# Optimization experiments

Measured on AMD Instinct MI355X. Metric: run time of the kernel, lower is better.

The kernel has to match this reference:

```python
import jax, jax.numpy as jnp
import numpy as np

B, D, O = 16384, 1024, 2048
MU, LAM = 0.9, 0.1


def setup_inputs() -> dict:
    key = jax.random.key(0)
    ks = jax.random.split(key, 16)
    stdv = float(1.0 / np.sqrt(D))
    u = lambda k, shape, s: jax.random.uniform(k, shape, jnp.float32, -s, s)
    return {
        "x": jax.random.normal(ks[0], (B, D), jnp.float32),
        "x_ctx": jax.random.normal(ks[1], (B, D), jnp.float32),
        "classifier": u(ks[2], (O, D), stdv),
        "none_tensor": u(ks[3], (1, D), stdv),
        "ctx_q_w": u(ks[4], (O, D), stdv),
        "ctx_q_b": u(ks[5], (O,), stdv),
        "word_g_w": u(ks[6], (1, D), stdv),
        "word_g_b": u(ks[7], (1,), stdv),
        "tcq_w1": u(ks[8], (D, D), stdv),
        "tcq_b1": u(ks[9], (D,), stdv),
        "tcq_w2": u(ks[10], (O, D), stdv),
        "tcq_b2": u(ks[11], (O,), stdv),
        "history_input": 0.1 * jax.random.normal(ks[12], (O - 1, D), jnp.float32),
        "history_count": jax.random.randint(ks[13], (O - 1,), 0, 10),
        "labels": jax.random.randint(ks[14], (B,), 0, O),
    }


def reference(x, x_ctx, classifier, none_tensor, ctx_q_w, ctx_q_b,
              word_g_w, word_g_b, tcq_w1, tcq_b1, tcq_w2, tcq_b2,
              history_input, history_count, labels):
    mu, lam = MU, LAM
    # ---- update_history (torch.no_grad), vectorized over classes via segment_sum ----
    xs = jax.lax.stop_gradient(x)
    sums = jax.ops.segment_sum(xs, labels, num_segments=O)               # [O, D]
    counts = jax.ops.segment_sum(jnp.ones((B,), jnp.float32), labels, num_segments=O)  # [O]
    has = counts[1:] > 0                                                  # classes 1..O-1
    cls_mean = sums[1:] / jnp.maximum(counts[1:], 1.0)[:, None]
    hist = jnp.where(has[:, None], mu * history_input + cls_mean, history_input)
    cnt = history_count + has.astype(history_count.dtype)
    # ---- generate_substitute (mu < 1 branch) ----
    denom = 1.0 - jnp.power(mu, jnp.maximum(cnt, 1).astype(jnp.float32))[:, None]
    v = hist * (1.0 - mu) / denom                                        # [O-1, D]
    r_sub = jnp.concatenate([none_tensor, v], axis=0)                    # [O, D]
    ctx_logits = x_ctx @ ctx_q_w.T + ctx_q_b                              # [B, O]
    att_logits = jax.nn.gelu(x @ tcq_w1.T + tcq_b1, approximate=False) @ tcq_w2.T + tcq_b2  # [B, O]
    # ---- gated combine + bilinear classifier (training=True path: w uses ctx_logits) ----
    g_word = jax.nn.sigmoid(x @ word_g_w.T + word_g_b)                    # [B, 1]
    w = g_word * jax.nn.sigmoid(ctx_logits)                               # [B, O]
    # logits = sum(((1-w)*x[:,None,:] + w*r_sub) * classifier, -1), collapsed algebraically
    logits = (1.0 - w) * (x @ classifier.T) + w * jnp.einsum('od,od->o', r_sub, classifier)[None, :]
    # ---- losses on labels >= 0 (mask-weighted means, jit-safe) ----
    mask = (labels >= 0).astype(jnp.float32)
    n = jnp.maximum(mask.sum(), 1.0)
    lsm = jax.nn.log_softmax(logits, axis=-1)
    nll = -jnp.take_along_axis(lsm, jnp.maximum(labels, 0)[:, None], axis=1)[:, 0]
    ce = (mask * nll).sum() / n
    mse_row = jnp.mean((ctx_logits - att_logits) ** 2, axis=-1)
    mse = (mask * mse_row).sum() / n
    return (ce + lam * mse, logits)
```

## Files before the change

kernel.cpp:

```cpp
#include <hip/hip_runtime.h>
#include <cstdint>
#include <cstddef>

#define DEV __device__ __forceinline__

typedef __attribute__((ext_vector_type(4))) float f32x4;
typedef __attribute__((ext_vector_type(8))) short bf16x8;
typedef unsigned short ushort_t;
typedef __attribute__((ext_vector_type(8))) unsigned short ushort8;

static constexpr int B_ = 16384, D_ = 1024, O_ = 2048;
static constexpr float LAM_ = 0.1f;

static constexpr size_t WS_XBF   = 0;
static constexpr size_t WS_XCBF  = WS_XBF   + (size_t)B_ * D_ * 2;
static constexpr size_t WS_HBF   = WS_XCBF  + (size_t)B_ * D_ * 2;
static constexpr size_t WS_CLSBF = WS_HBF   + (size_t)B_ * D_ * 2;
static constexpr size_t WS_CTWBF = WS_CLSBF + (size_t)O_ * D_ * 2;
static constexpr size_t WS_W2BF  = WS_CTWBF + (size_t)O_ * D_ * 2;
static constexpr size_t WS_W1BF  = WS_W2BF  + (size_t)O_ * D_ * 2;
static constexpr size_t WS_SMALL = WS_W1BF  + (size_t)D_ * D_ * 2;
static constexpr size_t SM_COUNTS = 0;
static constexpr size_t SM_TSUM   = 8192;
static constexpr size_t SM_MSE    = 16384;
static constexpr size_t SM_ZERO_BYTES = 82176;
static constexpr size_t SM_S      = 82176;
static constexpr size_t SM_GWORD  = 90368;
static constexpr size_t SM_CEROW  = 155904;

DEV float wave_sum(float v) {
  #pragma unroll
  for (int o = 32; o; o >>= 1) v += __shfl_xor(v, o, 64);
  return v;
}

DEV ushort_t f2bf1(float f) {
  union { float f; unsigned u; } c{f};
  unsigned r = c.u + 0x7fffu + ((c.u >> 16) & 1u);
  return (ushort_t)(r >> 16);
}

DEV float sigmoidf(float z) { return 1.0f / (1.0f + expf(-z)); }

DEV void gload_lds16(const ushort_t* g, ushort_t* l) {
  __builtin_amdgcn_global_load_lds((const __attribute__((address_space(1))) void*)g,
                                   (__attribute__((address_space(3))) void*)l, 16, 0, 0);
}

DEV void stage2(const ushort_t* __restrict__ s0, ushort_t* slot, int tid) {
  gload_lds16(s0, slot + tid * 8);
  gload_lds16(s0 + 128 * 1024, slot + (tid + 512) * 8);
}

DEV f32x4 mfma16(bf16x8 a, bf16x8 b, f32x4 c) {
  return __builtin_amdgcn_mfma_f32_16x16x32_bf16(a, b, c, 0, 0, 0);
}

#define DSR(dst, addr, off) \
  asm volatile("ds_read_b128 %0, %1 offset:" off : "=v"(dst) : "v"(addr))

__global__ __launch_bounds__(256) void f2bf_kernel(const float* __restrict__ in,
                                                   ushort_t* __restrict__ out, int n8) {
  int i = blockIdx.x * 256 + threadIdx.x;
  if (i >= n8) return;
  const float4* p = (const float4*)(in + (size_t)i * 8);
  float4 a = p[0], b = p[1];
  ushort8 o;
  o[0] = f2bf1(a.x); o[1] = f2bf1(a.y); o[2] = f2bf1(a.z); o[3] = f2bf1(a.w);
  o[4] = f2bf1(b.x); o[5] = f2bf1(b.y); o[6] = f2bf1(b.z); o[7] = f2bf1(b.w);
  *(ushort8*)(out + (size_t)i * 8) = o;
}

__global__ __launch_bounds__(256) void rowdot_kernel(const float* __restrict__ x,
    const float* __restrict__ cls, const float* __restrict__ wg,
    const float* __restrict__ wgb, const int* __restrict__ labels,
    float* __restrict__ tsum, float* __restrict__ counts, float* __restrict__ g_word) {
  int wave = threadIdx.x >> 6, lane = threadIdx.x & 63;
  int row = blockIdx.x * 4 + wave;
  const float* xr = x + (size_t)row * D_;
  int lab = labels[row];
  const float* cr = cls + (size_t)max(lab, 0) * D_;
  float t = 0.f, g = 0.f;
  #pragma unroll
  for (int j = 0; j < 4; ++j) {
    int d = j * 256 + lane * 4;
    float4 xv = *(const float4*)(xr + d);
    float4 cv = *(const float4*)(cr + d);
    float4 wv = *(const float4*)(wg + d);
    t += xv.x * cv.x + xv.y * cv.y + xv.z * cv.z + xv.w * cv.w;
    g += xv.x * wv.x + xv.y * wv.y + xv.z * wv.z + xv.w * wv.w;
  }
  t = wave_sum(t); g = wave_sum(g);
  if (lane == 0) {
    if (lab >= 0) {
      atomicAdd(&tsum[lab], t);
      atomicAdd(&counts[lab], 1.0f);
    }
    g_word[row] = sigmoidf(g + wgb[0]);
  }
}

__global__ __launch_bounds__(256) void scls_kernel(const float* __restrict__ cls,
    const float* __restrict__ none_t, const float* __restrict__ hist,
    const int* __restrict__ hcnt, const float* __restrict__ counts,
    const float* __restrict__ tsum, float* __restrict__ s) {
  int wave = threadIdx.x >> 6, lane = threadIdx.x & 63;
  int o = blockIdx.x * 4 + wave;
  if (o >= O_) return;
  const float* cr = cls + (size_t)o * D_;
  const float* src = (o == 0) ? none_t : hist + (size_t)(o - 1) * D_;
  float dv = 0.f;
  #pragma unroll
  for (int j = 0; j < 4; ++j) {
    int d = j * 256 + lane * 4;
    float4 a = *(const float4*)(src + d);
    float4 c = *(const float4*)(cr + d);
    dv += a.x * c.x + a.y * c.y + a.z * c.z + a.w * c.w;
  }
  dv = wave_sum(dv);
  if (lane == 0) {
    if (o == 0) { s[0] = dv; }
    else {
      float co = counts[o];
      bool has = co > 0.f;
      int cnt = hcnt[o - 1] + (has ? 1 : 0);
      float denom = 1.f - powf(0.9f, (float)max(cnt, 1));
      float val = has ? (0.9f * dv + tsum[o] / fmaxf(co, 1.f)) : dv;
      s[o] = (0.1f / denom) * val;
    }
  }
}

template<bool S01, bool S23, int W1, int W3>
DEV void tile8(int t, const ushort_t* __restrict__ sA0, const ushort_t* __restrict__ sB0,
               ushort_t* lds, int tid, unsigned aoffB, unsigned boffB, f32x4 (&acc)[8][4]) {
  const unsigned s0 = (unsigned)(((2 * t) & 3) * 16384);
  const unsigned s1 = (unsigned)(((2 * t + 1) & 3) * 16384);
  unsigned aA0 = aoffB + s0, aB0 = boffB + 65536u + s0;
  unsigned aA1 = aoffB + s1, aB1 = boffB + 65536u + s1;
  bf16x8 afr[4], bfr[4];
  DSR(bfr[0], aB0, "0"); DSR(bfr[1], aB0, "1024"); DSR(bfr[2], aB0, "2048"); DSR(bfr[3], aB0, "3072");
  DSR(afr[0], aA0, "0"); DSR(afr[1], aA0, "1024"); DSR(afr[2], aA0, "2048"); DSR(afr[3], aA0, "3072");
  if constexpr (S01) stage2(sA0 + (size_t)(2 * t + 3) * 32, lds + ((2 * t + 3) & 3) * 8192, tid);
  __builtin_amdgcn_s_barrier();
  asm volatile("s_waitcnt lgkmcnt(0)");
  __builtin_amdgcn_sched_barrier(0);
  __builtin_amdgcn_s_setprio(1);
  #pragma unroll
  for (int m = 0; m < 4; m++)
    #pragma unroll
    for (int n = 0; n < 4; n++) acc[m][n] = mfma16(afr[m], bfr[n], acc[m][n]);
  __builtin_amdgcn_s_setprio(0);
  __builtin_amdgcn_s_barrier();
  DSR(afr[0], aA0, "4096"); DSR(afr[1], aA0, "5120"); DSR(afr[2], aA0, "6144"); DSR(afr[3], aA0, "7168");
  if constexpr (S01) stage2(sB0 + (size_t)(2 * t + 3) * 32, lds + 32768 + ((2 * t + 3) & 3) * 8192, tid);
  __builtin_amdgcn_s_barrier();
  asm volatile("s_waitcnt lgkmcnt(0)");
  __builtin_amdgcn_sched_barrier(0);
  __builtin_amdgcn_s_setprio(1);
  #pragma unroll
  for (int m = 0; m < 4; m++)
    #pragma unroll
    for (int n = 0; n < 4; n++) acc[m + 4][n] = mfma16(afr[m], bfr[n], acc[m + 4][n]);
  __builtin_amdgcn_s_setprio(0);
  if constexpr (W1 == 8) asm volatile("s_waitcnt vmcnt(8)" ::: "memory");
  else if constexpr (W1 == 4) asm volatile("s_waitcnt vmcnt(4)" ::: "memory");
  else if constexpr (W1 == 0) asm volatile("s_waitcnt vmcnt(0)" ::: "memory");
  __builtin_amdgcn_s_barrier();
  DSR(bfr[0], aB1, "0"); DSR(bfr[1], aB1, "1024"); DSR(bfr[2], aB1, "2048"); DSR(bfr[3], aB1, "3072");
  DSR(afr[0], aA1, "0"); DSR(afr[1], aA1, "1024"); DSR(afr[2], aA1, "2048"); DSR(afr[3], aA1, "3072");
  if constexpr (S23) stage2(sA0 + (size_t)(2 * t + 4) * 32, lds + ((2 * t + 4) & 3) * 8192, tid);
  __builtin_amdgcn_s_barrier();
  asm volatile("s_waitcnt lgkmcnt(0)");
  __builtin_amdgcn_sched_barrier(0);
  __builtin_amdgcn_s_setprio(1);
  #pragma unroll
  for (int m = 0; m < 4; m++)
    #pragma unroll
    for (int n = 0; n < 4; n++) acc[m][n] = mfma16(afr[m], bfr[n], acc[m][n]);
  __builtin_amdgcn_s_setprio(0);
  __builtin_amdgcn_s_barrier();
  DSR(afr[0], aA1, "4096"); DSR(afr[1], aA1, "5120"); DSR(afr[2], aA1, "6144"); DSR(afr[3], aA1, "7168");
  if constexpr (S23) stage2(sB0 + (size_t)(2 * t + 4) * 32, lds + 32768 + ((2 * t + 4) & 3) * 8192, tid);
  __builtin_amdgcn_s_barrier();
  asm volatile("s_waitcnt lgkmcnt(0)");
  __builtin_amdgcn_sched_barrier(0);
  __builtin_amdgcn_s_setprio(1);
  #pragma unroll
  for (int m = 0; m < 4; m++)
    #pragma unroll
    for (int n = 0; n < 4; n++) acc[m + 4][n] = mfma16(afr[m], bfr[n], acc[m + 4][n]);
  __builtin_amdgcn_s_setprio(0);
  if constexpr (W3 == 8) asm volatile("s_waitcnt vmcnt(8)" ::: "memory");
  else if constexpr (W3 == 4) asm volatile("s_waitcnt vmcnt(4)" ::: "memory");
  else if constexpr (W3 == 2) asm volatile("s_waitcnt vmcnt(2)" ::: "memory");
  else if constexpr (W3 == 0) asm volatile("s_waitcnt vmcnt(0)" ::: "memory");
  __builtin_amdgcn_s_barrier();
}

template<int EPI, int NTSHIFT>
__global__ __launch_bounds__(512, 2) void gemm8_kernel(
    const ushort_t* __restrict__ A, const ushort_t* __restrict__ Bmat,
    const float* __restrict__ bias, float* __restrict__ fout,
    ushort_t* __restrict__ hout, const float* __restrict__ g_word,
    const float* __restrict__ svec, float* __restrict__ mse_row) {
  __shared__ __align__(16) ushort_t lds[65536];
  const int tid = threadIdx.x, lane = tid & 63, wave = tid >> 6;
  const int wr = wave >> 2, wc = wave & 3;
  const int nwg = 64 << NTSHIFT, cpx = nwg >> 3;
  int bid = blockIdx.x;
  int wg = (bid & 7) * cpx + (bid >> 3);
  const int bm = wg >> NTSHIFT, bn = wg & ((1 << NTSHIFT) - 1);
  const int NCOL = 256 << NTSHIFT;
  const int qsrc = (tid & 3) ^ ((tid >> 3) & 3);
  const ushort_t* sA0 = A + ((size_t)bm * 256 + (tid >> 2)) * 1024 + qsrc * 8;
  const ushort_t* sB0 = Bmat + ((size_t)bn * 256 + (tid >> 2)) * 1024 + qsrc * 8;
  const int qrd = (lane >> 4) ^ (((lane & 15) >> 1) & 3);
  const unsigned aoffB = (unsigned)(((wr * 128 + (lane & 15)) * 32 + qrd * 8) * 2);
  const unsigned boffB = (unsigned)(((wc * 64 + (lane & 15)) * 32 + qrd * 8) * 2);
  f32x4 acc[8][4] = {};
  stage2(sA0, lds, tid);
  stage2(sB0, lds + 32768, tid);
  stage2(sA0 + 32, lds + 8192, tid);
  stage2(sB0 + 32, lds + 32768 + 8192, tid);
  stage2(sA0 + 64, lds + 2 * 8192, tid);
  stage2(sB0 + 64, lds + 32768 + 2 * 8192, tid);
  asm volatile("s_waitcnt vmcnt(8)" ::: "memory");
  __builtin_amdgcn_s_barrier();
  for (int t = 0; t < 14; ++t)
    tile8<true, true, 8, 8>(t, sA0, sB0, lds, tid, aoffB, boffB, acc);
  tile8<true, false, 8, 4>(14, sA0, sB0, lds, tid, aoffB, boffB, acc);
  tile8<false, false, 0, 0>(15, sA0, sB0, lds, tid, aoffB, boffB, acc);
  #pragma unroll
  for (int m = 0; m < 8; m++) {
    #pragma unroll
    for (int i = 0; i < 4; i++) {
      int row = bm * 256 + wr * 128 + m * 16 + (lane >> 4) * 4 + i;
      float gw = 0.f, msum = 0.f;
      if constexpr (EPI == 3) gw = g_word[row];
      #pragma unroll
      for (int n = 0; n < 4; n++) {
        int col = bn * 256 + wc * 64 + n * 16 + (lane & 15);
        float v = acc[m][n][i];
        if constexpr (EPI == 0) {
          float z = v + bias[col];
          float gl = 0.5f * z * (1.f + erff(z * 0.70710678118f));
          hout[(size_t)row * 1024 + col] = f2bf1(gl);
        } else if constexpr (EPI == 1) {
          fout[(size_t)row * NCOL + col] = v + bias[col];
        } else if constexpr (EPI == 2) {
          float att = v + bias[col];
          float ctx = fout[(size_t)row * NCOL + col];
          float d = ctx - att;
          msum += d * d;
        } else {
          size_t off = (size_t)row * NCOL + col;
          float ctx = fout[off];
          float w = gw * sigmoidf(ctx);
          fout[off] = (1.f - w) * v + w * svec[col];
        }
      }
      if constexpr (EPI == 2) {
        #pragma unroll
        for (int o = 1; o < 16; o <<= 1) msum += __shfl_xor(msum, o, 64);
        if ((lane & 15) == 0) atomicAdd(&mse_row[row], msum);
      }
    }
  }
}

__global__ __launch_bounds__(256) void ce_kernel(const float* __restrict__ logits,
    const int* __restrict__ labels, float* __restrict__ ce_row) {
  int row = blockIdx.x, t = threadIdx.x, lane = t & 63, wave = t >> 6;
  const float* lr = logits + (size_t)row * O_;
  float v[8];
  float m = -INFINITY;
  #pragma unroll
  for (int j = 0; j < 8; j++) { v[j] = lr[t + j * 256]; m = fmaxf(m, v[j]); }
  #pragma unroll
  for (int o = 32; o; o >>= 1) m = fmaxf(m, __shfl_xor(m, o, 64));
  __shared__ float red[8];
  if (lane == 0) red[wave] = m;
  __syncthreads();
  m = fmaxf(fmaxf(red[0], red[1]), fmaxf(red[2], red[3]));
  float se = 0.f;
  #pragma unroll
  for (int j = 0; j < 8; j++) se += expf(v[j] - m);
  se = wave_sum(se);
  if (lane == 0) red[4 + wave] = se;
  __syncthreads();
  if (t == 0) {
    float bs = red[4] + red[5] + red[6] + red[7];
    int lab = labels[row];
    float nll = 0.f;
    if (lab >= 0) nll = -(lr[lab] - m - logf(bs));
    ce_row[row] = nll;
  }
}

__global__ __launch_bounds__(256) void finalize_kernel(const float* __restrict__ ce_row,
    const float* __restrict__ mse_row, const int* __restrict__ labels,
    float* __restrict__ out0) {
  int t = threadIdx.x, lane = t & 63, wave = t >> 6;
  float sn = 0.f, sm = 0.f, sc = 0.f;
  for (int i = t; i < B_; i += 256) {
    if (labels[i] >= 0) { sn += ce_row[i]; sm += mse_row[i]; sc += 1.f; }
  }
  sn = wave_sum(sn); sm = wave_sum(sm); sc = wave_sum(sc);
  __shared__ float r0[4], r1[4], r2[4];
  if (lane == 0) { r0[wave] = sn; r1[wave] = sm; r2[wave] = sc; }
  __syncthreads();
  if (t == 0) {
    float a = r0[0] + r0[1] + r0[2] + r0[3];
    float b = r1[0] + r1[1] + r1[2] + r1[3];
    float c = r2[0] + r2[1] + r2[2] + r2[3];
    out0[0] = (a + LAM_ * (b / (float)O_)) / fmaxf(c, 1.f);
  }
}

extern "C" void kernel_launch(void* const* d_in, const int* in_sizes, int n_in,
                              void* d_out, int out_size, void* d_ws, size_t ws_size,
                              hipStream_t stream) {
  const float* x        = (const float*)d_in[0];
  const float* x_ctx    = (const float*)d_in[1];
  const float* cls      = (const float*)d_in[2];
  const float* none_t   = (const float*)d_in[3];
  const float* ctx_q_w  = (const float*)d_in[4];
  const float* ctx_q_b  = (const float*)d_in[5];
  const float* word_g_w = (const float*)d_in[6];
  const float* word_g_b = (const float*)d_in[7];
  const float* w1       = (const float*)d_in[8];
  const float* b1       = (const float*)d_in[9];
  const float* w2       = (const float*)d_in[10];
  const float* b2       = (const float*)d_in[11];
  const float* hist     = (const float*)d_in[12];
  const int*   hcnt     = (const int*)d_in[13];
  const int*   labels   = (const int*)d_in[14];

  float* out  = (float*)d_out;
  float* out1 = out + 1;
  char* ws = (char*)d_ws;

  ushort_t* xbf   = (ushort_t*)(ws + WS_XBF);
  ushort_t* xcbf  = (ushort_t*)(ws + WS_XCBF);
  ushort_t* hbf   = (ushort_t*)(ws + WS_HBF);
  ushort_t* clsbf = (ushort_t*)(ws + WS_CLSBF);
  ushort_t* ctwbf = (ushort_t*)(ws + WS_CTWBF);
  ushort_t* w2bf  = (ushort_t*)(ws + WS_W2BF);
  ushort_t* w1bf  = (ushort_t*)(ws + WS_W1BF);
  float* counts   = (float*)(ws + WS_SMALL + SM_COUNTS);
  float* tsum     = (float*)(ws + WS_SMALL + SM_TSUM);
  float* mse_row  = (float*)(ws + WS_SMALL + SM_MSE);
  float* s        = (float*)(ws + WS_SMALL + SM_S);
  float* g_word   = (float*)(ws + WS_SMALL + SM_GWORD);
  float* ce_row   = (float*)(ws + WS_SMALL + SM_CEROW);

  hipMemsetAsync(ws + WS_SMALL, 0, SM_ZERO_BYTES, stream);

  f2bf_kernel<<<8192, 256, 0, stream>>>(x, xbf, B_ * D_ / 8);
  f2bf_kernel<<<8192, 256, 0, stream>>>(x_ctx, xcbf, B_ * D_ / 8);
  f2bf_kernel<<<1024, 256, 0, stream>>>(cls, clsbf, O_ * D_ / 8);
  f2bf_kernel<<<1024, 256, 0, stream>>>(ctx_q_w, ctwbf, O_ * D_ / 8);
  f2bf_kernel<<<1024, 256, 0, stream>>>(w2, w2bf, O_ * D_ / 8);
  f2bf_kernel<<<512, 256, 0, stream>>>(w1, w1bf, D_ * D_ / 8);

  rowdot_kernel<<<B_ / 4, 256, 0, stream>>>(x, cls, word_g_w, word_g_b, labels,
                                            tsum, counts, g_word);
  scls_kernel<<<O_ / 4, 256, 0, stream>>>(cls, none_t, hist, hcnt, counts, tsum, s);

  gemm8_kernel<0, 2><<<64 * 4, 512, 0, stream>>>(xbf, w1bf, b1, nullptr, hbf,
                                                 nullptr, nullptr, nullptr);
  gemm8_kernel<1, 3><<<64 * 8, 512, 0, stream>>>(xcbf, ctwbf, ctx_q_b, out1, nullptr,
                                                 nullptr, nullptr, nullptr);
  gemm8_kernel<2, 3><<<64 * 8, 512, 0, stream>>>(hbf, w2bf, b2, out1, nullptr,
                                                 nullptr, nullptr, mse_row);
  gemm8_kernel<3, 3><<<64 * 8, 512, 0, stream>>>(xbf, clsbf, nullptr, out1, nullptr,
                                                 g_word, s, nullptr);

  ce_kernel<<<B_, 256, 0, stream>>>(out1, labels, ce_row);
  finalize_kernel<<<1, 256, 0, stream>>>(ce_row, mse_row, labels, out);
}
```

Measured before the change: 466.8 us.

## Double-buffer LDS fragment registers to overlap ds_reads with MFMA in GEMM

Restructures the GEMM inner loop so LDS fragment reads for the next sub-step are issued before the current MFMA block, using two register buffers for A and B fragments. Partial lgkmcnt waits replace full drains, and one barrier per phase is removed. The vmcnt waits are retuned for the new schedule. This is meant to hide LDS read latency behind matrix math, at the cost of more VGPRs and a more delicate ordering that could hit races or spills.

Result: faster. 455.0 us (-2.5%).

```diff
diff --git a/kernel.cpp b/kernel.cpp
--- a/kernel.cpp
+++ b/kernel.cpp
@@ -59,6 +59,14 @@
 #define DSR(dst, addr, off) \
   asm volatile("ds_read_b128 %0, %1 offset:" off : "=v"(dst) : "v"(addr))
 
+template<int N> DEV void wait_vm() {
+  if constexpr (N == 8)      asm volatile("s_waitcnt vmcnt(8)" ::: "memory");
+  else if constexpr (N == 6) asm volatile("s_waitcnt vmcnt(6)" ::: "memory");
+  else if constexpr (N == 4) asm volatile("s_waitcnt vmcnt(4)" ::: "memory");
+  else if constexpr (N == 2) asm volatile("s_waitcnt vmcnt(2)" ::: "memory");
+  else                       asm volatile("s_waitcnt vmcnt(0)" ::: "memory");
+}
+
 __global__ __launch_bounds__(256) void f2bf_kernel(const float* __restrict__ in,
                                                    ushort_t* __restrict__ out, int n8) {
   int i = blockIdx.x * 256 + threadIdx.x;
@@ -131,70 +139,78 @@
   }
 }
 
-template<bool S01, bool S23, int W1, int W3>
-DEV void tile8(int t, const ushort_t* __restrict__ sA0, const ushort_t* __restrict__ sB0,
-               ushort_t* lds, int tid, unsigned aoffB, unsigned boffB, f32x4 (&acc)[8][4]) {
-  const unsigned s0 = (unsigned)(((2 * t) & 3) * 16384);
-  const unsigned s1 = (unsigned)(((2 * t + 1) & 3) * 16384);
-  unsigned aA0 = aoffB + s0, aB0 = boffB + 65536u + s0;
-  unsigned aA1 = aoffB + s1, aB1 = boffB + 65536u + s1;
-  bf16x8 afr[4], bfr[4];
-  DSR(bfr[0], aB0, "0"); DSR(bfr[1], aB0, "1024"); DSR(bfr[2], aB0, "2048"); DSR(bfr[3], aB0, "3072");
-  DSR(afr[0], aA0, "0"); DSR(afr[1], aA0, "1024"); DSR(afr[2], aA0, "2048"); DSR(afr[3], aA0, "3072");
+template<bool S01, bool S23, int W0, int W1, int W2, int W3, bool RLAST>
+DEV void tile4(int t, const ushort_t* __restrict__ sA0, const ushort_t* __restrict__ sB0,
+               ushort_t* lds, int tid, unsigned aoffB, unsigned boffB,
+               bf16x8 (&bA)[2][4], bf16x8 (&bB)[2][4], f32x4 (&acc)[8][4]) {
+  const unsigned sl0 = (unsigned)(((2 * t) & 3) * 16384);
+  const unsigned sl1 = (unsigned)(((2 * t + 1) & 3) * 16384);
+  const unsigned sl2 = (unsigned)(((2 * t + 2) & 3) * 16384);
+  const unsigned aA0 = aoffB + sl0;
+  const unsigned aA1 = aoffB + sl1, aB1 = boffB + 65536u + sl1;
+  const unsigned aA2 = aoffB + sl2, aB2 = boffB + 65536u + sl2;
+  DSR(bA[1][0], aA0, "4096"); DSR(bA[1][1], aA0, "5120");
+  DSR(bA[1][2], aA0, "6144"); DSR(bA[1][3], aA0, "7168");
   if constexpr (S01) stage2(sA0 + (size_t)(2 * t + 3) * 32, lds + ((2 * t + 3) & 3) * 8192, tid);
-  __builtin_amdgcn_s_barrier();
-  asm volatile("s_waitcnt lgkmcnt(0)");
+  asm volatile("s_waitcnt lgkmcnt(4)");
   __builtin_amdgcn_sched_barrier(0);
   __builtin_amdgcn_s_setprio(1);
   #pragma unroll
   for (int m = 0; m < 4; m++)
     #pragma unroll
-    for (int n = 0; n < 4; n++) acc[m][n] = mfma16(afr[m], bfr[n], acc[m][n]);
+    for (int n = 0; n < 4; n++) acc[m][n] = mfma16(bA[0][m], bB[0][n], acc[m][n]);
   __builtin_amdgcn_s_setprio(0);
+  __builtin_amdgcn_sched_barrier(0);
+  wait_vm<W0>();
   __builtin_amdgcn_s_barrier();
-  DSR(afr[0], aA0, "4096"); DSR(afr[1], aA0, "5120"); DSR(afr[2], aA0, "6144"); DSR(afr[3], aA0, "7168");
+  DSR(bB[1][0], aB1, "0"); DSR(bB[1][1], aB1, "1024");
+  DSR(bB[1][2], aB1, "2048"); DSR(bB[1][3], aB1, "3072");
+  DSR(bA[0][0], aA1, "0"); DSR(bA[0][1], aA1, "1024");
+  DSR(bA[0][2], aA1, "2048"); DSR(bA[0][3], aA1, "3072");
   if constexpr (S01) stage2(sB0 + (size_t)(2 * t + 3) * 32, lds + 32768 + ((2 * t + 3) & 3) * 8192, tid);
-  __builtin_amdgcn_s_barrier();
-  asm volatile("s_waitcnt lgkmcnt(0)");
+  asm volatile("s_waitcnt lgkmcnt(8)");
   __builtin_amdgcn_sched_barrier(0);
   __builtin_amdgcn_s_setprio(1);
   #pragma unroll
   for (int m = 0; m < 4; m++)
     #pragma unroll
-    for (int n = 0; n < 4; n++) acc[m + 4][n] = mfma16(afr[m], bfr[n], acc[m + 4][n]);
+    for (int n = 0; n < 4; n++) acc[m + 4][n] = mfma16(bA[1][m], bB[0][n], acc[m + 4][n]);
   __builtin_amdgcn_s_setprio(0);
-  if constexpr (W1 == 8) asm volatile("s_waitcnt vmcnt(8)" ::: "memory");
-  else if constexpr (W1 == 4) asm volatile("s_waitcnt vmcnt(4)" ::: "memory");
-  else if constexpr (W1 == 0) asm volatile("s_waitcnt vmcnt(0)" ::: "memory");
+  __builtin_amdgcn_sched_barrier(0);
+  wait_vm<W1>();
   __builtin_amdgcn_s_barrier();
-  DSR(bfr[0], aB1, "0"); DSR(bfr[1], aB1, "1024"); DSR(bfr[2], aB1, "2048"); DSR(bfr[3], aB1, "3072");
-  DSR(afr[0], aA1, "0"); DSR(afr[1], aA1, "1024"); DSR(afr[2], aA1, "2048"); DSR(afr[3], aA1, "3072");
+  DSR(bA[1][0], aA1, "4096"); DSR(bA[1][1], aA1, "5120");
+  DSR(bA[1][2], aA1, "6144"); DSR(bA[1][3], aA1, "7168");
   if constexpr (S23) stage2(sA0 + (size_t)(2 * t + 4) * 32, lds + ((2 * t + 4) & 3) * 8192, tid);
-  __builtin_amdgcn_s_barrier();
-  asm volatile("s_waitcnt lgkmcnt(0)");
+  asm volatile("s_waitcnt lgkmcnt(4)");
   __builtin_amdgcn_sched_barrier(0);
   __builtin_amdgcn_s_setprio(1);
   #pragma unroll
   for (int m = 0; m < 4; m++)
     #pragma unroll
-    for (int n = 0; n < 4; n++) acc[m][n] = mfma16(afr[m], bfr[n], acc[m][n]);
+    for (int n = 0; n < 4; n++) acc[m][n] = mfma16(bA[0][m], bB[1][n], acc[m][n]);
   __builtin_amdgcn_s_setprio(0);
+  __builtin_amdgcn_sched_barrier(0);
+  wait_vm<W2>();
   __builtin_amdgcn_s_barrier();
-  DSR(afr[0], aA1, "4096"); DSR(afr[1], aA1, "5120"); DSR(afr[2], aA1, "6144"); DSR(afr[3], aA1, "7168");
+  if constexpr (!RLAST) {
+    DSR(bB[0][0], aB2, "0"); DSR(bB[0][1], aB2, "1024");
+    DSR(bB[0][2], aB2, "2048"); DSR(bB[0][3], aB2, "3072");
+    DSR(bA[0][0], aA2, "0"); DSR(bA[0][1], aA2, "1024");
+    DSR(bA[0][2], aA2, "2048"); DSR(bA[0][3], aA2, "3072");
+  }
   if constexpr (S23) stage2(sB0 + (size_t)(2 * t + 4) * 32, lds + 32768 + ((2 * t + 4) & 3) * 8192, tid);
-  __builtin_amdgcn_s_barrier();
-  asm volatile("s_waitcnt lgkmcnt(0)");
+  if constexpr (RLAST) asm volatile("s_waitcnt lgkmcnt(0)");
+  else                 asm volatile("s_waitcnt lgkmcnt(8)");
   __builtin_amdgcn_sched_barrier(0);
   __builtin_amdgcn_s_setprio(1);
   #pragma unroll
   for (int m = 0; m < 4; m++)
     #pragma unroll
-    for (int n = 0; n < 4; n++) acc[m + 4][n] = mfma16(afr[m], bfr[n], acc[m + 4][n]);
+    for (int n = 0; n < 4; n++) acc[m + 4][n] = mfma16(bA[1][m], bB[1][n], acc[m + 4][n]);
   __builtin_amdgcn_s_setprio(0);
-  if constexpr (W3 == 8) asm volatile("s_waitcnt vmcnt(8)" ::: "memory");
-  else if constexpr (W3 == 4) asm volatile("s_waitcnt vmcnt(4)" ::: "memory");
-  else if constexpr (W3 == 2) asm volatile("s_waitcnt vmcnt(2)" ::: "memory");
-  else if constexpr (W3 == 0) asm volatile("s_waitcnt vmcnt(0)" ::: "memory");
+  __builtin_amdgcn_sched_barrier(0);
+  wait_vm<W3>();
   __builtin_amdgcn_s_barrier();
 }
 
@@ -227,10 +243,18 @@
   stage2(sB0 + 64, lds + 32768 + 2 * 8192, tid);
   asm volatile("s_waitcnt vmcnt(8)" ::: "memory");
   __builtin_amdgcn_s_barrier();
+  bf16x8 bA[2][4], bB[2][4];
+  {
+    const unsigned aB0 = boffB + 65536u;
+    DSR(bB[0][0], aB0, "0"); DSR(bB[0][1], aB0, "1024");
+    DSR(bB[0][2], aB0, "2048"); DSR(bB[0][3], aB0, "3072");
+    DSR(bA[0][0], aoffB, "0"); DSR(bA[0][1], aoffB, "1024");
+    DSR(bA[0][2], aoffB, "2048"); DSR(bA[0][3], aoffB, "3072");
+  }
   for (int t = 0; t < 14; ++t)
-    tile8<true, true, 8, 8>(t, sA0, sB0, lds, tid, aoffB, boffB, acc);
-  tile8<true, false, 8, 4>(14, sA0, sB0, lds, tid, aoffB, boffB, acc);
-  tile8<false, false, 0, 0>(15, sA0, sB0, lds, tid, aoffB, boffB, acc);
+    tile4<true, true, 6, 6, 6, 6, false>(t, sA0, sB0, lds, tid, aoffB, boffB, bA, bB, acc);
+  tile4<true, false, 6, 6, 4, 2, false>(14, sA0, sB0, lds, tid, aoffB, boffB, bA, bB, acc);
+  tile4<false, false, 0, 0, 0, 0, true>(15, sA0, sB0, lds, tid, aoffB, boffB, bA, bB, acc);
   #pragma unroll
   for (int m = 0; m < 8; m++) {
     #pragma unroll
```

## Shrink GEMM tile to 256x128 with 3-stage pipeline for higher occupancy

Applied to the files above, without the earlier changes.

Replaces the 256x256 block tile with a 4-stage LDS ring by a 256x128 tile, 4x2 wave layout and a 3-stage ring of single k-slices. LDS use drops from 128 KB to 72 KB and launch bounds rise to 4 blocks per CU, so more workgroups can overlap and the grids double. The cost is lower arithmetic intensity per tile, since A is reloaded twice as often, and fewer MFMAs between barriers.

Result: slower. 478.4 us (+2.5%).

```diff
diff --git a/kernel.cpp b/kernel.cpp
--- a/kernel.cpp
+++ b/kernel.cpp
@@ -47,11 +47,6 @@
                                    (__attribute__((address_space(3))) void*)l, 16, 0, 0);
 }
 
-DEV void stage2(const ushort_t* __restrict__ s0, ushort_t* slot, int tid) {
-  gload_lds16(s0, slot + tid * 8);
-  gload_lds16(s0 + 128 * 1024, slot + (tid + 512) * 8);
-}
-
 DEV f32x4 mfma16(bf16x8 a, bf16x8 b, f32x4 c) {
   return __builtin_amdgcn_mfma_f32_16x16x32_bf16(a, b, c, 0, 0, 0);
 }
@@ -131,116 +126,77 @@
   }
 }
 
-template<bool S01, bool S23, int W1, int W3>
-DEV void tile8(int t, const ushort_t* __restrict__ sA0, const ushort_t* __restrict__ sB0,
-               ushort_t* lds, int tid, unsigned aoffB, unsigned boffB, f32x4 (&acc)[8][4]) {
-  const unsigned s0 = (unsigned)(((2 * t) & 3) * 16384);
-  const unsigned s1 = (unsigned)(((2 * t + 1) & 3) * 16384);
-  unsigned aA0 = aoffB + s0, aB0 = boffB + 65536u + s0;
-  unsigned aA1 = aoffB + s1, aB1 = boffB + 65536u + s1;
-  bf16x8 afr[4], bfr[4];
-  DSR(bfr[0], aB0, "0"); DSR(bfr[1], aB0, "1024"); DSR(bfr[2], aB0, "2048"); DSR(bfr[3], aB0, "3072");
-  DSR(afr[0], aA0, "0"); DSR(afr[1], aA0, "1024"); DSR(afr[2], aA0, "2048"); DSR(afr[3], aA0, "3072");
-  if constexpr (S01) stage2(sA0 + (size_t)(2 * t + 3) * 32, lds + ((2 * t + 3) & 3) * 8192, tid);
-  __builtin_amdgcn_s_barrier();
-  asm volatile("s_waitcnt lgkmcnt(0)");
-  __builtin_amdgcn_sched_barrier(0);
-  __builtin_amdgcn_s_setprio(1);
-  #pragma unroll
-  for (int m = 0; m < 4; m++)
-    #pragma unroll
-    for (int n = 0; n < 4; n++) acc[m][n] = mfma16(afr[m], bfr[n], acc[m][n]);
-  __builtin_amdgcn_s_setprio(0);
-  __builtin_amdgcn_s_barrier();
-  DSR(afr[0], aA0, "4096"); DSR(afr[1], aA0, "5120"); DSR(afr[2], aA0, "6144"); DSR(afr[3], aA0, "7168");
-  if constexpr (S01) stage2(sB0 + (size_t)(2 * t + 3) * 32, lds + 32768 + ((2 * t + 3) & 3) * 8192, tid);
-  __builtin_amdgcn_s_barrier();
-  asm volatile("s_waitcnt lgkmcnt(0)");
-  __builtin_amdgcn_sched_barrier(0);
-  __builtin_amdgcn_s_setprio(1);
-  #pragma unroll
-  for (int m = 0; m < 4; m++)
-    #pragma unroll
-    for (int n = 0; n < 4; n++) acc[m + 4][n] = mfma16(afr[m], bfr[n], acc[m + 4][n]);
-  __builtin_amdgcn_s_setprio(0);
-  if constexpr (W1 == 8) asm volatile("s_waitcnt vmcnt(8)" ::: "memory");
-  else if constexpr (W1 == 4) asm volatile("s_waitcnt vmcnt(4)" ::: "memory");
-  else if constexpr (W1 == 0) asm volatile("s_waitcnt vmcnt(0)" ::: "memory");
-  __builtin_amdgcn_s_barrier();
-  DSR(bfr[0], aB1, "0"); DSR(bfr[1], aB1, "1024"); DSR(bfr[2], aB1, "2048"); DSR(bfr[3], aB1, "3072");
-  DSR(afr[0], aA1, "0"); DSR(afr[1], aA1, "1024"); DSR(afr[2], aA1, "2048"); DSR(afr[3], aA1, "3072");
-  if constexpr (S23) stage2(sA0 + (size_t)(2 * t + 4) * 32, lds + ((2 * t + 4) & 3) * 8192, tid);
-  __builtin_amdgcn_s_barrier();
-  asm volatile("s_waitcnt lgkmcnt(0)");
-  __builtin_amdgcn_sched_barrier(0);
-  __builtin_amdgcn_s_setprio(1);
-  #pragma unroll
-  for (int m = 0; m < 4; m++)
-    #pragma unroll
-    for (int n = 0; n < 4; n++) acc[m][n] = mfma16(afr[m], bfr[n], acc[m][n]);
-  __builtin_amdgcn_s_setprio(0);
-  __builtin_amdgcn_s_barrier();
-  DSR(afr[0], aA1, "4096"); DSR(afr[1], aA1, "5120"); DSR(afr[2], aA1, "6144"); DSR(afr[3], aA1, "7168");
-  if constexpr (S23) stage2(sB0 + (size_t)(2 * t + 4) * 32, lds + 32768 + ((2 * t + 4) & 3) * 8192, tid);
-  __builtin_amdgcn_s_barrier();
-  asm volatile("s_waitcnt lgkmcnt(0)");
-  __builtin_amdgcn_sched_barrier(0);
-  __builtin_amdgcn_s_setprio(1);
-  #pragma unroll
-  for (int m = 0; m < 4; m++)
-    #pragma unroll
-    for (int n = 0; n < 4; n++) acc[m + 4][n] = mfma16(afr[m], bfr[n], acc[m + 4][n]);
-  __builtin_amdgcn_s_setprio(0);
-  if constexpr (W3 == 8) asm volatile("s_waitcnt vmcnt(8)" ::: "memory");
-  else if constexpr (W3 == 4) asm volatile("s_waitcnt vmcnt(4)" ::: "memory");
-  else if constexpr (W3 == 2) asm volatile("s_waitcnt vmcnt(2)" ::: "memory");
-  else if constexpr (W3 == 0) asm volatile("s_waitcnt vmcnt(0)" ::: "memory");
-  __builtin_amdgcn_s_barrier();
-}
-
-template<int EPI, int NTSHIFT>
-__global__ __launch_bounds__(512, 2) void gemm8_kernel(
+template<int EPI, int NBN>
+__global__ __launch_bounds__(512, 4) void gemm8_kernel(
     const ushort_t* __restrict__ A, const ushort_t* __restrict__ Bmat,
     const float* __restrict__ bias, float* __restrict__ fout,
     ushort_t* __restrict__ hout, const float* __restrict__ g_word,
     const float* __restrict__ svec, float* __restrict__ mse_row) {
-  __shared__ __align__(16) ushort_t lds[65536];
+  __shared__ __align__(16) ushort_t lds[36864];
   const int tid = threadIdx.x, lane = tid & 63, wave = tid >> 6;
-  const int wr = wave >> 2, wc = wave & 3;
-  const int nwg = 64 << NTSHIFT, cpx = nwg >> 3;
+  const int wr = wave >> 1, wc = wave & 1;
+  const int nwg = 64 * NBN, cpx = nwg >> 3;
   int bid = blockIdx.x;
   int wg = (bid & 7) * cpx + (bid >> 3);
-  const int bm = wg >> NTSHIFT, bn = wg & ((1 << NTSHIFT) - 1);
-  const int NCOL = 256 << NTSHIFT;
+  const int bm = wg / NBN, bn = wg % NBN;
+  const int NCOL = NBN * 128;
   const int qsrc = (tid & 3) ^ ((tid >> 3) & 3);
   const ushort_t* sA0 = A + ((size_t)bm * 256 + (tid >> 2)) * 1024 + qsrc * 8;
-  const ushort_t* sB0 = Bmat + ((size_t)bn * 256 + (tid >> 2)) * 1024 + qsrc * 8;
+  const ushort_t* sB0 = Bmat + ((size_t)bn * 128 + (tid >> 2)) * 1024 + qsrc * 8;
   const int qrd = (lane >> 4) ^ (((lane & 15) >> 1) & 3);
-  const unsigned aoffB = (unsigned)(((wr * 128 + (lane & 15)) * 32 + qrd * 8) * 2);
-  const unsigned boffB = (unsigned)(((wc * 64 + (lane & 15)) * 32 + qrd * 8) * 2);
-  f32x4 acc[8][4] = {};
-  stage2(sA0, lds, tid);
-  stage2(sB0, lds + 32768, tid);
-  stage2(sA0 + 32, lds + 8192, tid);
-  stage2(sB0 + 32, lds + 32768 + 8192, tid);
-  stage2(sA0 + 64, lds + 2 * 8192, tid);
-  stage2(sB0 + 64, lds + 32768 + 2 * 8192, tid);
-  asm volatile("s_waitcnt vmcnt(8)" ::: "memory");
+  const unsigned aoffB = (unsigned)(((wr * 64 + (lane & 15)) * 32 + qrd * 8) * 2);
+  const unsigned boffB = (unsigned)(((wc * 64 + (lane & 15)) * 32 + qrd * 8) * 2) + 49152u;
+  f32x4 acc[4][4] = {};
+  gload_lds16(sA0, lds + tid * 8);
+  gload_lds16(sA0 + 128 * 1024, lds + (tid + 512) * 8);
+  gload_lds16(sB0, lds + 24576 + tid * 8);
+  gload_lds16(sA0 + 32, lds + 8192 + tid * 8);
+  gload_lds16(sA0 + 32 + 128 * 1024, lds + 8192 + (tid + 512) * 8);
+  gload_lds16(sB0 + 32, lds + 24576 + 4096 + tid * 8);
+  asm volatile("s_waitcnt vmcnt(3)" ::: "memory");
   __builtin_amdgcn_s_barrier();
-  for (int t = 0; t < 14; ++t)
-    tile8<true, true, 8, 8>(t, sA0, sB0, lds, tid, aoffB, boffB, acc);
-  tile8<true, false, 8, 4>(14, sA0, sB0, lds, tid, aoffB, boffB, acc);
-  tile8<false, false, 0, 0>(15, sA0, sB0, lds, tid, aoffB, boffB, acc);
-  #pragma unroll
-  for (int m = 0; m < 8; m++) {
+  #pragma unroll
+  for (int t = 0; t < 32; ++t) {
+    const unsigned aA = aoffB + (unsigned)((t % 3) * 16384);
+    const unsigned aB = boffB + (unsigned)((t % 3) * 8192);
+    bf16x8 fA[4], fB[4];
+    DSR(fB[0], aB, "0"); DSR(fB[1], aB, "1024");
+    DSR(fB[2], aB, "2048"); DSR(fB[3], aB, "3072");
+    DSR(fA[0], aA, "0"); DSR(fA[1], aA, "1024");
+    DSR(fA[2], aA, "2048"); DSR(fA[3], aA, "3072");
+    if (t < 30) {
+      const ushort_t* srcA = sA0 + (size_t)(t + 2) * 32;
+      const ushort_t* srcB = sB0 + (size_t)(t + 2) * 32;
+      ushort_t* dA = lds + ((t + 2) % 3) * 8192;
+      ushort_t* dB = lds + 24576 + ((t + 2) % 3) * 4096;
+      gload_lds16(srcA, dA + tid * 8);
+      gload_lds16(srcA + 128 * 1024, dA + (tid + 512) * 8);
+      gload_lds16(srcB, dB + tid * 8);
+    }
+    __builtin_amdgcn_s_barrier();
+    asm volatile("s_waitcnt lgkmcnt(0)");
+    __builtin_amdgcn_sched_barrier(0);
+    __builtin_amdgcn_s_setprio(1);
+    #pragma unroll
+    for (int m = 0; m < 4; m++)
+      #pragma unroll
+      for (int n = 0; n < 4; n++) acc[m][n] = mfma16(fA[m], fB[n], acc[m][n]);
+    __builtin_amdgcn_s_setprio(0);
+    __builtin_amdgcn_sched_barrier(0);
+    if (t < 30)      asm volatile("s_waitcnt vmcnt(3)" ::: "memory");
+    else if (t == 30) asm volatile("s_waitcnt vmcnt(0)" ::: "memory");
+    __builtin_amdgcn_s_barrier();
+  }
+  #pragma unroll
+  for (int m = 0; m < 4; m++) {
     #pragma unroll
     for (int i = 0; i < 4; i++) {
-      int row = bm * 256 + wr * 128 + m * 16 + (lane >> 4) * 4 + i;
+      int row = bm * 256 + wr * 64 + m * 16 + (lane >> 4) * 4 + i;
       float gw = 0.f, msum = 0.f;
       if constexpr (EPI == 3) gw = g_word[row];
       #pragma unroll
       for (int n = 0; n < 4; n++) {
-        int col = bn * 256 + wc * 64 + n * 16 + (lane & 15);
+        int col = bn * 128 + wc * 64 + n * 16 + (lane & 15);
         float v = acc[m][n][i];
         if constexpr (EPI == 0) {
           float z = v + bias[col];
@@ -368,14 +324,14 @@
                                             tsum, counts, g_word);
   scls_kernel<<<O_ / 4, 256, 0, stream>>>(cls, none_t, hist, hcnt, counts, tsum, s);
 
-  gemm8_kernel<0, 2><<<64 * 4, 512, 0, stream>>>(xbf, w1bf, b1, nullptr, hbf,
-                                                 nullptr, nullptr, nullptr);
-  gemm8_kernel<1, 3><<<64 * 8, 512, 0, stream>>>(xcbf, ctwbf, ctx_q_b, out1, nullptr,
-                                                 nullptr, nullptr, nullptr);
-  gemm8_kernel<2, 3><<<64 * 8, 512, 0, stream>>>(hbf, w2bf, b2, out1, nullptr,
-                                                 nullptr, nullptr, mse_row);
-  gemm8_kernel<3, 3><<<64 * 8, 512, 0, stream>>>(xbf, clsbf, nullptr, out1, nullptr,
-                                                 g_word, s, nullptr);
+  gemm8_kernel<0, 8><<<512, 512, 0, stream>>>(xbf, w1bf, b1, nullptr, hbf,
+                                              nullptr, nullptr, nullptr);
+  gemm8_kernel<1, 16><<<1024, 512, 0, stream>>>(xcbf, ctwbf, ctx_q_b, out1, nullptr,
+                                                nullptr, nullptr, nullptr);
+  gemm8_kernel<2, 16><<<1024, 512, 0, stream>>>(hbf, w2bf, b2, out1, nullptr,
+                                                nullptr, nullptr, mse_row);
+  gemm8_kernel<3, 16><<<1024, 512, 0, stream>>>(xbf, clsbf, nullptr, out1, nullptr,
+                                                g_word, s, nullptr);
 
   ce_kernel<<<B_, 256, 0, stream>>>(out1, labels, ce_row);
   finalize_kernel<<<1, 256, 0, stream>>>(ce_row, mse_row, labels, out);
```
